# Kernel tuning notes

Measured on AMD Instinct MI355X. Metric: run time of the kernel, lower is better.

## Reference

```python
import jax, jax.numpy as jnp
import numpy as np
from jax import lax

TWN_THRESHOLD_FACTOR = 0.05


def ternary_quantize(w, t):
    # codes in {-1, 0, +1}
    return (w > t).astype(w.dtype) - (w < -t).astype(w.dtype)


def setup_inputs() -> dict:
    key = jax.random.key(0)
    kx, kw, kb = jax.random.split(key, 3)
    x = jax.random.normal(kx, (32, 128, 56, 56), dtype=jnp.float32)
    weight = jax.random.normal(kw, (256, 128, 3, 3), dtype=jnp.float32)
    bias = jax.random.normal(kb, (256,), dtype=jnp.float32)
    return {"x": x, "weight": weight, "bias": bias}


def reference(x, weight, bias):
    # threshold from detached weights (matches weight.detach().abs().max())
    threshold = TWN_THRESHOLD_FACTOR * jnp.max(jnp.abs(lax.stop_gradient(weight)))
    q_weight = ternary_quantize(weight, threshold)
    out = lax.conv_general_dilated(
        x, q_weight,
        window_strides=(1, 1),
        padding="VALID",  # F.conv2d default padding=0
        dimension_numbers=("NCHW", "OIHW", "NCHW"),
    )
    return out + bias[None, :, None, None]
```

## Files before the change

kernel.cpp:

```cpp
#include <hip/hip_runtime.h>
#include <hip/hip_bf16.h>
#include <stdint.h>

#define NB   32
#define CIN  128
#define HIN  56
#define WIN  56
#define KOUT 256
#define HOUT 54
#define WOUT 54
#define PQ   (HOUT*WOUT)
#define NPIX (NB*PQ)
#define KK   (CIN*9)
#define HW   (HIN*WIN)
#define TWN_FACTOR 0.05f

typedef short bf16x8 __attribute__((ext_vector_type(8)));
typedef float f32x4  __attribute__((ext_vector_type(4)));

__device__ __forceinline__ void glds16(const void* g, void* l) {
  __builtin_amdgcn_global_load_lds(
      (__attribute__((address_space(1))) void*)(g),
      (__attribute__((address_space(3))) void*)(l),
      16, 0, 0);
}

__device__ __forceinline__ unsigned pack_bf16(float a, float b) {
  return (unsigned)__bfloat16_as_ushort(__float2bfloat16(a)) |
         ((unsigned)__bfloat16_as_ushort(__float2bfloat16(b)) << 16);
}

__global__ void prep_k(const float* __restrict__ x, const float4* __restrict__ w4,
                       float* __restrict__ amax, __hip_bfloat16* __restrict__ xt) {
  __shared__ __hip_bfloat16 tl[64 * 130 + 32];
  __shared__ float sm[4];
  int bid = blockIdx.x;
  int t   = threadIdx.x;

  if (bid < 288) {
    float4 v = w4[bid * 256 + t];
    float m = fmaxf(fmaxf(fabsf(v.x), fabsf(v.y)), fmaxf(fabsf(v.z), fabsf(v.w)));
    #pragma unroll
    for (int off = 32; off > 0; off >>= 1)
      m = fmaxf(m, __shfl_down(m, off));
    int lane = t & 63, wv = t >> 6;
    if (lane == 0) sm[wv] = m;
    __syncthreads();
    if (t == 0)
      atomicMax(amax, fmaxf(fmaxf(sm[0], sm[1]), fmaxf(sm[2], sm[3])));
    return;
  }

  int b2 = bid - 288;
  int n  = b2 / 49, pc = b2 - n * 49;
  const float* xb = x + (size_t)n * CIN * HW + pc * 64;
  int f4  = t & 15;
  int cp0 = t >> 4;
  #pragma unroll
  for (int rd = 0; rd < 4; ++rd) {
    int cp = cp0 + rd * 16;
    const float* s0 = xb + (size_t)(2 * cp) * HW + f4 * 4;
    float4 v0 = *(const float4*)(s0);
    float4 v1 = *(const float4*)(s0 + HW);
    *(unsigned*)&tl[(f4 * 4 + 0) * 130 + 2 * cp] = pack_bf16(v0.x, v1.x);
    *(unsigned*)&tl[(f4 * 4 + 1) * 130 + 2 * cp] = pack_bf16(v0.y, v1.y);
    *(unsigned*)&tl[(f4 * 4 + 2) * 130 + 2 * cp] = pack_bf16(v0.z, v1.z);
    *(unsigned*)&tl[(f4 * 4 + 3) * 130 + 2 * cp] = pack_bf16(v0.w, v1.w);
  }
  __syncthreads();
  int cc = t & 15, p0 = t >> 4;
  __hip_bfloat16* op = xt + ((size_t)n * HW + pc * 64) * CIN + cc * 8;
  #pragma unroll
  for (int p = p0; p < 64; p += 16)
    *(bf16x8*)(op + (size_t)p * CIN) = *(const bf16x8*)&tl[p * 130 + cc * 8];
}

__global__ void quant_k(const float* __restrict__ w, const float* __restrict__ amax,
                        __hip_bfloat16* __restrict__ qA) {
  float thr = TWN_FACTOR * (*amax);
  int t  = blockIdx.x * 256 + threadIdx.x;
  int kc = t >> 8, row = t & 255;
  int rs = kc >> 4, c0 = (kc & 15) << 3;
  bf16x8 q;
  #pragma unroll
  for (int j = 0; j < 8; ++j) {
    float v  = w[(size_t)(row * CIN + c0 + j) * 9 + rs];
    float qq = (v > thr) ? 1.f : ((v < -thr) ? -1.f : 0.f);
    q[j] = (short)__bfloat16_as_ushort(__float2bfloat16(qq));
  }
  *(bf16x8*)(qA + (size_t)t * 8) = q;
}

__global__ __launch_bounds__(256, 4) void conv_gemm(
    const __hip_bfloat16* __restrict__ xt,
    const __hip_bfloat16* __restrict__ qA,
    const float* __restrict__ bias,
    float* __restrict__ out) {
  __shared__ __hip_bfloat16 Bs[2][128 * 64];

  const int tid  = threadIdx.x;
  const int wave = tid >> 6;
  const int lane = tid & 63;
  const int quad = lane >> 4;
  const int l16  = lane & 15;

  const int orig = blockIdx.x;
  const int xcd  = orig & 7;
  const int loc  = orig >> 3;
  const int bid  = (xcd < 2) ? xcd * 183 + loc
                             : 366 + (xcd - 2) * 182 + loc;

  const int ktile = bid & 1;
  const int ptile = bid >> 1;
  const int k0    = ktile * 128;
  const int pbase = ptile * 128;

  const int wm = (wave >> 1) * 64;
  const int wn = (wave & 1) * 64;

  const int r8 = lane >> 3;
  const int ch = lane & 7;
  unsigned boffm[4];
  #pragma unroll
  for (int m = 0; m < 4; ++m) {
    int row  = wave * 32 + m * 8 + r8;
    int prow = pbase + row;
    int n = prow / PQ; int rm = prow - n * PQ;
    int p = rm / WOUT; int q = rm - p * WOUT;
    boffm[m] = (unsigned)(n * HW + p * WIN + q) * CIN + ((ch ^ (row & 7)) << 3);
  }

  unsigned aoff[4];
  #pragma unroll
  for (int i = 0; i < 4; ++i)
    aoff[i] = (unsigned)(quad * 256 + (k0 + wm + i * 16 + l16)) * 8;

  f32x4 acc[4][4];
  #pragma unroll
  for (int i = 0; i < 4; ++i)
    #pragma unroll
    for (int j = 0; j < 4; ++j)
      acc[i][j] = (f32x4){0.f, 0.f, 0.f, 0.f};

  {
    char* bdst0 = (char*)Bs + wave * 4096;
    #pragma unroll
    for (int m = 0; m < 4; ++m)
      glds16(xt + boffm[m], bdst0 + m * 1024);
  }

  #pragma unroll
  for (int t = 0; t < 18; ++t) {
    __syncthreads();

    if (t < 17) {
      const int tn  = t + 1;
      const int rsn = tn >> 1;
      const int rn  = rsn / 3, sn = rsn - rn * 3;
      const unsigned bst = (unsigned)((rn * WIN + sn) * CIN + (tn & 1) * 64);
      char* bdst = (char*)Bs + (unsigned)(tn & 1) * 16384 + wave * 4096;
      #pragma unroll
      for (int m = 0; m < 4; ++m)
        glds16(xt + boffm[m] + bst, bdst + m * 1024);
    }
    __builtin_amdgcn_sched_barrier(0);

    const unsigned astep = ((unsigned)(t >> 1) * 16 + (unsigned)(t & 1) * 8) * 2048;
    const char* bp = (const char*)Bs + (unsigned)(t & 1) * 16384;
    #pragma unroll
    for (int h = 0; h < 2; ++h) {
      bf16x8 af[4], bfr[4];
      #pragma unroll
      for (int i = 0; i < 4; ++i)
        af[i] = *(const bf16x8*)(qA + aoff[i] + astep + (unsigned)h * 4 * 2048);
      #pragma unroll
      for (int i = 0; i < 4; ++i) {
        int row = wn + i * 16 + l16;
        bfr[i] = *(const bf16x8*)(bp + (row * 64 + (((h * 4 + quad) ^ (row & 7)) << 3)) * 2);
      }
      #pragma unroll
      for (int i = 0; i < 4; ++i)
        #pragma unroll
        for (int j = 0; j < 4; ++j)
          acc[i][j] = __builtin_amdgcn_mfma_f32_16x16x32_bf16(af[i], bfr[j], acc[i][j], 0, 0, 0);
    }
  }

  __syncthreads();

  {
    float* Sw = (float*)Bs + wave * 2048;
    const int ST  = 65;
    const int rk  = lane >> 3;
    const int rp  = (lane & 7) * 4;
    const float4* b4 = (const float4*)bias;

    #pragma unroll
    for (int i = 0; i < 4; ++i) {
      float4 bv = b4[(k0 + wm + i * 16 + quad * 4) >> 2];
      #pragma unroll
      for (int j = 0; j < 4; ++j) {
        Sw[(quad * 4 + 0) * ST + j * 16 + l16] = acc[i][j][0] + bv.x;
        Sw[(quad * 4 + 1) * ST + j * 16 + l16] = acc[i][j][1] + bv.y;
        Sw[(quad * 4 + 2) * ST + j * 16 + l16] = acc[i][j][2] + bv.z;
        Sw[(quad * 4 + 3) * ST + j * 16 + l16] = acc[i][j][3] + bv.w;
      }
      asm volatile("s_waitcnt lgkmcnt(0)" ::: "memory");
      __builtin_amdgcn_sched_barrier(0);
      #pragma unroll
      for (int ri = 0; ri < 2; ++ri) {
        int klocal = ri * 8 + rk;
        int k = k0 + wm + i * 16 + klocal;
        #pragma unroll
        for (int cg = 0; cg < 2; ++cg) {
          int pixl = cg * 32 + rp;
          float4 v = *(const float4*)&Sw[klocal * ST + pixl];
          int pix = pbase + wn + pixl;
          int n = pix / PQ, pq = pix - n * PQ;
          *(float4*)(out + (size_t)n * (KOUT * PQ) + (size_t)k * PQ + pq) = v;
        }
      }
      asm volatile("s_waitcnt lgkmcnt(0)" ::: "memory");
      __builtin_amdgcn_sched_barrier(0);
    }
  }
}

extern "C" void kernel_launch(void* const* d_in, const int* in_sizes, int n_in,
                              void* d_out, int out_size, void* d_ws, size_t ws_size,
                              hipStream_t stream) {
  const float* x    = (const float*)d_in[0];
  const float* w    = (const float*)d_in[1];
  const float* bias = (const float*)d_in[2];
  float* out = (float*)d_out;

  float* amax = (float*)d_ws;
  __hip_bfloat16* xt = (__hip_bfloat16*)((char*)d_ws + 256);
  __hip_bfloat16* qA = (__hip_bfloat16*)((char*)d_ws + 256 + (size_t)NB * HW * CIN * 2);

  prep_k  <<<dim3(1856), dim3(256), 0, stream>>>(x, (const float4*)w, amax, xt);
  quant_k <<<dim3(144),  dim3(256), 0, stream>>>(w, amax, qA);
  conv_gemm<<<dim3(1458), dim3(256), 0, stream>>>(xt, qA, bias, out);
}
```

Before: 212.4 us.

## Merge K tiles into 512-thread blocks sharing one pixel tile with ping-pong MFMA scheduling

Each block now covers all 256 output channels for a 128-pixel tile, using 8 waves instead of 4. The activation tile is loaded into LDS once and shared by both channel halves, which halves the redundant global-to-LDS traffic. The main loop is restructured: A fragments are loaded up front, MFMAs are split into two halves separated by a barrier, and s_setprio raises wave priority during compute so waves interleave. Risks include lower occupancy, more barrier overhead, and removal of the full unroll of the t loop.

```diff
diff --git a/kernel.cpp b/kernel.cpp
--- a/kernel.cpp
+++ b/kernel.cpp
@@ -91,12 +91,12 @@
   *(bf16x8*)(qA + (size_t)t * 8) = q;
 }
 
-__global__ __launch_bounds__(256, 4) void conv_gemm(
+__global__ __launch_bounds__(512, 2) void conv_gemm(
     const __hip_bfloat16* __restrict__ xt,
     const __hip_bfloat16* __restrict__ qA,
     const float* __restrict__ bias,
     float* __restrict__ out) {
-  __shared__ __hip_bfloat16 Bs[2][128 * 64];
+  __shared__ char smem[65536];
 
   const int tid  = threadIdx.x;
   const int wave = tid >> 6;
@@ -104,36 +104,33 @@
   const int quad = lane >> 4;
   const int l16  = lane & 15;
 
+  const int wvm = wave >> 1;
+  const int wvn = wave & 1;
+  const int km  = wvm * 64;
+  const int wn  = wvn * 64;
+
   const int orig = blockIdx.x;
   const int xcd  = orig & 7;
   const int loc  = orig >> 3;
-  const int bid  = (xcd < 2) ? xcd * 183 + loc
-                             : 366 + (xcd - 2) * 182 + loc;
-
-  const int ktile = bid & 1;
-  const int ptile = bid >> 1;
-  const int k0    = ktile * 128;
+  const int ptile = (xcd < 1) ? loc : 92 + (xcd - 1) * 91 + loc;
   const int pbase = ptile * 128;
-
-  const int wm = (wave >> 1) * 64;
-  const int wn = (wave & 1) * 64;
 
   const int r8 = lane >> 3;
   const int ch = lane & 7;
-  unsigned boffm[4];
-  #pragma unroll
-  for (int m = 0; m < 4; ++m) {
-    int row  = wave * 32 + m * 8 + r8;
+  unsigned boffm[2];
+  #pragma unroll
+  for (int g = 0; g < 2; ++g) {
+    int row  = wave * 16 + g * 8 + r8;
     int prow = pbase + row;
     int n = prow / PQ; int rm = prow - n * PQ;
     int p = rm / WOUT; int q = rm - p * WOUT;
-    boffm[m] = (unsigned)(n * HW + p * WIN + q) * CIN + ((ch ^ (row & 7)) << 3);
+    boffm[g] = (unsigned)(n * HW + p * WIN + q) * CIN + ((unsigned)(ch ^ (row & 7)) << 3);
   }
 
   unsigned aoff[4];
   #pragma unroll
   for (int i = 0; i < 4; ++i)
-    aoff[i] = (unsigned)(quad * 256 + (k0 + wm + i * 16 + l16)) * 8;
+    aoff[i] = (unsigned)(quad * 256 + (km + i * 16 + l16)) * 8;
 
   f32x4 acc[4][4];
   #pragma unroll
@@ -143,53 +140,79 @@
       acc[i][j] = (f32x4){0.f, 0.f, 0.f, 0.f};
 
   {
-    char* bdst0 = (char*)Bs + wave * 4096;
-    #pragma unroll
-    for (int m = 0; m < 4; ++m)
-      glds16(xt + boffm[m], bdst0 + m * 1024);
-  }
-
-  #pragma unroll
+    char* bdst = smem + wave * 2048;
+    #pragma unroll
+    for (int g = 0; g < 2; ++g)
+      glds16(xt + boffm[g], bdst + g * 1024);
+  }
+
   for (int t = 0; t < 18; ++t) {
-    __syncthreads();
+    asm volatile("s_waitcnt vmcnt(0)" ::: "memory");
+    __builtin_amdgcn_s_barrier();
+    __builtin_amdgcn_sched_barrier(0);
+
+    const unsigned astep = ((unsigned)(t >> 1) * 16 + (unsigned)(t & 1) * 8) * 2048;
+    bf16x8 af[8];
+    #pragma unroll
+    for (int i = 0; i < 4; ++i)
+      #pragma unroll
+      for (int h = 0; h < 2; ++h)
+        af[i * 2 + h] = *(const bf16x8*)(qA + aoff[i] + astep + (unsigned)h * 4 * 2048);
+    __builtin_amdgcn_sched_barrier(0);
 
     if (t < 17) {
       const int tn  = t + 1;
       const int rsn = tn >> 1;
       const int rn  = rsn / 3, sn = rsn - rn * 3;
       const unsigned bst = (unsigned)((rn * WIN + sn) * CIN + (tn & 1) * 64);
-      char* bdst = (char*)Bs + (unsigned)(tn & 1) * 16384 + wave * 4096;
-      #pragma unroll
-      for (int m = 0; m < 4; ++m)
-        glds16(xt + boffm[m] + bst, bdst + m * 1024);
+      char* bdst = smem + (unsigned)(tn & 1) * 16384 + wave * 2048;
+      #pragma unroll
+      for (int g = 0; g < 2; ++g)
+        glds16(xt + boffm[g] + bst, bdst + g * 1024);
     }
     __builtin_amdgcn_sched_barrier(0);
 
-    const unsigned astep = ((unsigned)(t >> 1) * 16 + (unsigned)(t & 1) * 8) * 2048;
-    const char* bp = (const char*)Bs + (unsigned)(t & 1) * 16384;
-    #pragma unroll
-    for (int h = 0; h < 2; ++h) {
-      bf16x8 af[4], bfr[4];
-      #pragma unroll
-      for (int i = 0; i < 4; ++i)
-        af[i] = *(const bf16x8*)(qA + aoff[i] + astep + (unsigned)h * 4 * 2048);
-      #pragma unroll
-      for (int i = 0; i < 4; ++i) {
-        int row = wn + i * 16 + l16;
-        bfr[i] = *(const bf16x8*)(bp + (row * 64 + (((h * 4 + quad) ^ (row & 7)) << 3)) * 2);
+    const char* bp = smem + (unsigned)(t & 1) * 16384;
+    bf16x8 xf[8];
+    #pragma unroll
+    for (int j = 0; j < 4; ++j)
+      #pragma unroll
+      for (int h = 0; h < 2; ++h) {
+        int row = wn + j * 16 + l16;
+        xf[j * 2 + h] =
+            *(const bf16x8*)(bp + row * 128 + (((h * 4 + quad) ^ (row & 7)) << 4));
       }
-      #pragma unroll
-      for (int i = 0; i < 4; ++i)
+    asm volatile("s_waitcnt lgkmcnt(0)" ::: "memory");
+    __builtin_amdgcn_sched_barrier(0);
+
+    __builtin_amdgcn_s_setprio(1);
+    #pragma unroll
+    for (int i = 0; i < 2; ++i)
+      #pragma unroll
+      for (int h = 0; h < 2; ++h)
         #pragma unroll
         for (int j = 0; j < 4; ++j)
-          acc[i][j] = __builtin_amdgcn_mfma_f32_16x16x32_bf16(af[i], bfr[j], acc[i][j], 0, 0, 0);
-    }
+          acc[i][j] = __builtin_amdgcn_mfma_f32_16x16x32_bf16(af[i * 2 + h], xf[j * 2 + h],
+                                                              acc[i][j], 0, 0, 0);
+    __builtin_amdgcn_s_setprio(0);
+    __builtin_amdgcn_s_barrier();
+
+    __builtin_amdgcn_s_setprio(1);
+    #pragma unroll
+    for (int i = 2; i < 4; ++i)
+      #pragma unroll
+      for (int h = 0; h < 2; ++h)
+        #pragma unroll
+        for (int j = 0; j < 4; ++j)
+          acc[i][j] = __builtin_amdgcn_mfma_f32_16x16x32_bf16(af[i * 2 + h], xf[j * 2 + h],
+                                                              acc[i][j], 0, 0, 0);
+    __builtin_amdgcn_s_setprio(0);
   }
 
   __syncthreads();
 
   {
-    float* Sw = (float*)Bs + wave * 2048;
+    float* Sw = (float*)smem + wave * 2048;
     const int ST  = 65;
     const int rk  = lane >> 3;
     const int rp  = (lane & 7) * 4;
@@ -197,7 +220,7 @@
 
     #pragma unroll
     for (int i = 0; i < 4; ++i) {
-      float4 bv = b4[(k0 + wm + i * 16 + quad * 4) >> 2];
+      float4 bv = b4[(km + i * 16 + quad * 4) >> 2];
       #pragma unroll
       for (int j = 0; j < 4; ++j) {
         Sw[(quad * 4 + 0) * ST + j * 16 + l16] = acc[i][j][0] + bv.x;
@@ -210,7 +233,7 @@
       #pragma unroll
       for (int ri = 0; ri < 2; ++ri) {
         int klocal = ri * 8 + rk;
-        int k = k0 + wm + i * 16 + klocal;
+        int k = km + i * 16 + klocal;
         #pragma unroll
         for (int cg = 0; cg < 2; ++cg) {
           int pixl = cg * 32 + rp;
@@ -240,5 +263,5 @@
 
   prep_k  <<<dim3(1856), dim3(256), 0, stream>>>(x, (const float4*)w, amax, xt);
   quant_k <<<dim3(144),  dim3(256), 0, stream>>>(w, amax, qA);
-  conv_gemm<<<dim3(1458), dim3(256), 0, stream>>>(xt, qA, bias, out);
-}
+  conv_gemm<<<dim3(729), dim3(512), 0, stream>>>(xt, qA, bias, out);
+}
```

Result: slower. 224.8 us (+5.8%).
